# Performance work log

Hardware: AMD Instinct MI355X
Metric: run time of the kernel (lower is better)

Reference implementation:

```python
import jax, jax.numpy as jnp
import numpy as np

N = 50000      # nodes
E = 800000     # edges (avg degree 16)
IN = 128; HID = 128; OUT = 128; HEADS = 4
NEG_SLOPE = 0.2


def setup_inputs() -> dict:
    key = jax.random.key(0)
    ks = jax.random.split(key, 16)
    def glorot(k, shape):
        fan = shape[0] if len(shape) == 2 else int(np.prod(shape))
        return jax.random.normal(k, shape, jnp.float32) * np.float32(1.0 / np.sqrt(fan))
    C = HID // HEADS
    x = jax.random.normal(ks[0], (N, IN), jnp.float32)
    edge_index = jax.random.randint(ks[1], (2, E), 0, N, jnp.int32)
    return {
        "x": x, "edge_index": edge_index,
        "W1": glorot(ks[2], (IN, HID)),  "as1": glorot(ks[3], (HEADS, C)),  "ad1": glorot(ks[4], (HEADS, C)),  "b1": jnp.zeros((HID,), jnp.float32),
        "W2": glorot(ks[5], (HID, HID)), "as2": glorot(ks[6], (HEADS, C)),  "ad2": glorot(ks[7], (HEADS, C)),  "b2": jnp.zeros((HID,), jnp.float32),
        "W3": glorot(ks[8], (HID, OUT)), "as3": glorot(ks[9], (1, OUT)),    "ad3": glorot(ks[10], (1, OUT)),   "b3": jnp.zeros((OUT,), jnp.float32),
    }


def gat_conv(x, ei, W, a_src, a_dst, b, concat):
    # x: [N,Fin], ei: [2,E'] (self-loops included), W: [Fin, H*C], a_*: [H,C]
    n = x.shape[0]
    H, C = a_src.shape
    h = (x @ W).reshape(n, H, C)                         # [N,H,C]
    src, dst = ei[0], ei[1]
    alpha_s = jnp.einsum('nhc,hc->nh', h, a_src)         # [N,H]
    alpha_d = jnp.einsum('nhc,hc->nh', h, a_dst)
    e = jax.nn.leaky_relu(alpha_s[src] + alpha_d[dst], NEG_SLOPE)  # [E',H]
    # segment softmax over destination neighborhoods
    m = jax.ops.segment_max(e, dst, num_segments=n)      # [N,H]
    p = jnp.exp(e - m[dst])
    denom = jax.ops.segment_sum(p, dst, num_segments=n)  # [N,H]
    alpha = p / (denom[dst] + 1e-16)                     # [E',H]
    out = jax.ops.segment_sum(h[src] * alpha[:, :, None], dst, num_segments=n)  # [N,H,C]
    out = out.reshape(n, H * C) if concat else out.mean(axis=1)
    return out + b


def reference(x, edge_index, W1, as1, ad1, b1, W2, as2, ad2, b2, W3, as3, ad3, b3):
    n = x.shape[0]
    loops = jnp.arange(n, dtype=edge_index.dtype)
    ei = jnp.concatenate([edge_index, jnp.stack([loops, loops])], axis=1)  # add self-loops
    h = jax.nn.relu(gat_conv(x, ei, W1, as1, ad1, b1, True))   # dropout p=0 / eval: identity
    h = jax.nn.relu(gat_conv(h, ei, W2, as2, ad2, b2, True))
    return gat_conv(h, ei, W3, as3, ad3, b3, False)
```

## Files before the change

kernel.cpp:

```cpp
#include <hip/hip_runtime.h>
#include <hip/hip_bf16.h>
#include <math.h>

#define GB 512
#define SCB 2048

typedef __attribute__((ext_vector_type(8))) short bf16x8;
typedef __attribute__((ext_vector_type(4))) float f32x4;

__device__ __forceinline__ float lrelu(float v) { return fmaxf(v, 0.2f * v); }

__device__ __forceinline__ unsigned fenc(float f) {
    unsigned u = __float_as_uint(f);
    return (u & 0x80000000u) ? ~u : (u | 0x80000000u);
}
__device__ __forceinline__ float fdec(unsigned u) {
    return __uint_as_float((u & 0x80000000u) ? (u & 0x7FFFFFFFu) : ~u);
}
__device__ __forceinline__ unsigned short f2bf(float f) {
    union { __hip_bfloat16 b; unsigned short u; } cv;
    cv.b = __float2bfloat16(f);
    return cv.u;
}
__device__ __forceinline__ float bflo(unsigned u) { return __uint_as_float(u << 16); }
__device__ __forceinline__ float bfhi(unsigned u) { return __uint_as_float(u & 0xFFFF0000u); }


__global__ void setup_scatter(const float* __restrict__ x,
                              const float* __restrict__ W1, const float* __restrict__ W2,
                              const float* __restrict__ W3,
                              unsigned short* __restrict__ xb,
                              unsigned short* __restrict__ Wt1, unsigned short* __restrict__ Wt2,
                              unsigned short* __restrict__ Wt3,
                              int* __restrict__ cnt, unsigned short* __restrict__ srcs,
                              unsigned* __restrict__ gmax, unsigned short* __restrict__ hb,
                              const int* __restrict__ ei, int E,
                              int N, int GX, int pn) {
    int b = blockIdx.x, t = threadIdx.x;
    if (b < GX) {
        int i = b * 256 + t;
        if (i < N * 32) {
            float4 v = ((const float4*)x)[i];
            ushort4 o;
            o.x = f2bf(v.x); o.y = f2bf(v.y); o.z = f2bf(v.z); o.w = f2bf(v.w);
            ((ushort4*)xb)[i] = o;
        }
        if (i < N) srcs[(size_t)i << 6] = (unsigned short)i;
        if (i < 12) gmax[i] = fenc(-1e30f);
        if (i < 64) ((unsigned*)hb)[(size_t)N * 64 + i] = 0;
        return;
    }
    if (b < GX + 192) {
        int j = (b - GX) * 256 + t;
        int mm = j >> 14, e = j & 16383;
        const float* W = (mm == 0) ? W1 : (mm == 1) ? W2 : W3;
        unsigned short* Wt = (mm == 0) ? Wt1 : (mm == 1) ? Wt2 : Wt3;
        int k = e >> 7, c = e & 127;
        Wt[c * 128 + k] = f2bf(W[e]);
        return;
    }
    {
        int sb = b - GX - 192;
        int part = sb & 7;
        int chunk = sb >> 3;
        int stride = (SCB >> 3) * 256;
        int lo = part * pn, hi = min(lo + pn, N);
        for (int i = chunk * 256 + t; i < E; i += stride) {
            int d = ei[E + i];
            if (d >= lo && d < hi) {
                int idx = 1 + atomicAdd(&cnt[d], 1);
                if (idx < 64) srcs[((size_t)d << 6) + idx] = (unsigned short)ei[i];
            }
        }
    }
}


__device__ __forceinline__ void pad_body(int pb, int t, int* __restrict__ cnt,
                                         unsigned short* __restrict__ srcs, int N) {
    int n = pb * 256 + t;
    if (n >= N) return;
    int dr = cnt[n] + 1;
    if (dr > 64) dr = 64;
    int q = (dr + 3) >> 2;
    for (int k = dr; k < q * 4; k++) srcs[((size_t)n << 6) + k] = (unsigned short)N;
    cnt[n] = q;
}


template <int H>
__device__ __forceinline__ void gemm_body2(int wid, int nwaves, int wave,
                                           const unsigned short* __restrict__ xb,
                                           const unsigned short* __restrict__ Wt,
                                           const float* __restrict__ a_s,
                                           const float* __restrict__ a_d,
                                           unsigned short* __restrict__ hb,
                                           float* __restrict__ asb,
                                           float* __restrict__ adb,
                                           unsigned* __restrict__ gmax,
                                           float* __restrict__ wlds,
                                           float (*smax)[4], int N) {
    constexpr int HH = (H == 4) ? 4 : 1;
    int lane = threadIdx.x & 63;
    int lrow = lane & 15;
    int kg = lane >> 4;

    bf16x8 B[32];
#pragma unroll
    for (int ct = 0; ct < 8; ct++)
#pragma unroll
        for (int kk = 0; kk < 4; kk++)
            B[ct * 4 + kk] = *(const bf16x8*)(Wt + (size_t)(ct * 16 + lrow) * 128 + kk * 32 + kg * 8);

    int ntiles = (N + 15) >> 4;
    float wmax = -1e30f;

    bf16x8 A[4];
    {
        int tt = (wid < ntiles) ? wid : 0;
        int arow = min(tt * 16 + lrow, N - 1);
        const bf16x8* ap = (const bf16x8*)(xb + (size_t)arow * 128 + kg * 8);
        A[0] = ap[0]; A[1] = ap[4]; A[2] = ap[8]; A[3] = ap[12];
    }

    for (int t = wid; t < ntiles; t += nwaves) {
        bf16x8 An[4];
        {
            int tn = (t + nwaves < ntiles) ? t + nwaves : t;
            int arow = min(tn * 16 + lrow, N - 1);
            const bf16x8* ap = (const bf16x8*)(xb + (size_t)arow * 128 + kg * 8);
            An[0] = ap[0]; An[1] = ap[4]; An[2] = ap[8]; An[3] = ap[12];
        }
        f32x4 acc[8];
#pragma unroll
        for (int ct = 0; ct < 8; ct++) acc[ct] = (f32x4)0.f;
#pragma unroll
        for (int kk = 0; kk < 4; kk++)
#pragma unroll
            for (int ct = 0; ct < 8; ct++)
                acc[ct] = __builtin_amdgcn_mfma_f32_16x16x32_bf16(A[kk], B[ct * 4 + kk], acc[ct], 0, 0, 0);

#pragma unroll
        for (int ct = 0; ct < 8; ct++)
#pragma unroll
            for (int reg = 0; reg < 4; reg++)
                wlds[(kg * 4 + reg) * 132 + ct * 16 + lrow] = acc[ct][reg];

        const float* rp = wlds + lrow * 132 + kg * 32;
        const float* asp = a_s + kg * 32;
        const float* adp = a_d + kg * 32;
        float hv[32];
        float s = 0.f, d = 0.f;
#pragma unroll
        for (int q = 0; q < 8; q++) {
            float4 v = *(const float4*)(rp + q * 4);
            float4 av = *(const float4*)(asp + q * 4);
            float4 dv = *(const float4*)(adp + q * 4);
            hv[q * 4 + 0] = v.x; hv[q * 4 + 1] = v.y; hv[q * 4 + 2] = v.z; hv[q * 4 + 3] = v.w;
            s += v.x * av.x + v.y * av.y + v.z * av.z + v.w * av.w;
            d += v.x * dv.x + v.y * dv.y + v.z * dv.z + v.w * dv.w;
        }
        if (H == 1) {
            s += __shfl_xor(s, 16); s += __shfl_xor(s, 32);
            d += __shfl_xor(d, 16); d += __shfl_xor(d, 32);
        }
        int r = t * 16 + lrow;
        bool valid = r < N;
        if (valid) {
            if (H == 4) {
                asb[(size_t)r * 4 + kg] = s;
                adb[(size_t)r * 4 + kg] = d;
            } else if (kg == 0) {
                asb[r] = s;
                adb[r] = d;
            }
        }
        wmax = fmaxf(wmax, valid ? s : -1e30f);
        unsigned st[16];
#pragma unroll
        for (int q = 0; q < 16; q++)
            st[q] = (unsigned)f2bf(hv[2 * q]) | ((unsigned)f2bf(hv[2 * q + 1]) << 16);
        if (valid) {
            uint4* dst = (uint4*)(hb + (size_t)r * 128 + kg * 32);
            uint4 s0; s0.x = st[0];  s0.y = st[1];  s0.z = st[2];  s0.w = st[3];
            uint4 s1; s1.x = st[4];  s1.y = st[5];  s1.z = st[6];  s1.w = st[7];
            uint4 s2; s2.x = st[8];  s2.y = st[9];  s2.z = st[10]; s2.w = st[11];
            uint4 s3; s3.x = st[12]; s3.y = st[13]; s3.z = st[14]; s3.w = st[15];
            dst[0] = s0; dst[1] = s1; dst[2] = s2; dst[3] = s3;
        }
#pragma unroll
        for (int q = 0; q < 4; q++) A[q] = An[q];
    }

    if (H == 4) {
        wmax = fmaxf(wmax, __shfl_xor(wmax, 1));
        wmax = fmaxf(wmax, __shfl_xor(wmax, 2));
        wmax = fmaxf(wmax, __shfl_xor(wmax, 4));
        wmax = fmaxf(wmax, __shfl_xor(wmax, 8));
        if (lrow == 0) smax[wave][kg] = wmax;
    } else {
        wmax = fmaxf(wmax, __shfl_xor(wmax, 1));
        wmax = fmaxf(wmax, __shfl_xor(wmax, 2));
        wmax = fmaxf(wmax, __shfl_xor(wmax, 4));
        wmax = fmaxf(wmax, __shfl_xor(wmax, 8));
        wmax = fmaxf(wmax, __shfl_xor(wmax, 16));
        wmax = fmaxf(wmax, __shfl_xor(wmax, 32));
        if (lane == 0) smax[wave][0] = wmax;
    }
    __syncthreads();
    if (threadIdx.x < HH) {
        float m = fmaxf(fmaxf(smax[0][threadIdx.x], smax[1][threadIdx.x]),
                        fmaxf(smax[2][threadIdx.x], smax[3][threadIdx.x]));
        atomicMax(&gmax[threadIdx.x], fenc(m));
    }
    if (wid == 0 && threadIdx.x == 0) {
#pragma unroll
        for (int hd = 0; hd < HH; hd++) asb[(size_t)N * H + hd] = -1e30f;
    }
}


__global__ __launch_bounds__(256, 2) void gemm1_k(const unsigned short* __restrict__ xb,
                                                  const unsigned short* __restrict__ Wt,
                                                  const float* __restrict__ a_s,
                                                  const float* __restrict__ a_d,
                                                  unsigned short* __restrict__ hb,
                                                  float* __restrict__ asb,
                                                  float* __restrict__ adb,
                                                  unsigned* __restrict__ gmax, int N) {
    __shared__ float lds[4][16 * 132];
    __shared__ float smax[4][4];
    int wave = threadIdx.x >> 6;
    gemm_body2<4>(blockIdx.x * 4 + wave, GB * 4, wave, xb, Wt, a_s, a_d,
                  hb, asb, adb, gmax, lds[wave], smax, N);
}

__global__ __launch_bounds__(256, 2) void gemm2_pad(const unsigned short* __restrict__ xb,
                                                    const unsigned short* __restrict__ Wt,
                                                    const float* __restrict__ a_s,
                                                    const float* __restrict__ a_d,
                                                    unsigned short* __restrict__ hb,
                                                    float* __restrict__ asb,
                                                    float* __restrict__ adb,
                                                    unsigned* __restrict__ gmax,
                                                    int* __restrict__ cnt,
                                                    unsigned short* __restrict__ srcs, int N) {
    __shared__ float lds[4][16 * 132];
    __shared__ float smax[4][4];
    if ((int)blockIdx.x < GB) {
        int wave = threadIdx.x >> 6;
        gemm_body2<4>(blockIdx.x * 4 + wave, GB * 4, wave, xb, Wt, a_s, a_d,
                      hb, asb, adb, gmax, lds[wave], smax, N);
    } else {
        pad_body(blockIdx.x - GB, threadIdx.x, cnt, srcs, N);
    }
}

__global__ __launch_bounds__(256, 2) void gemm3_k(const unsigned short* __restrict__ xb,
                                                  const unsigned short* __restrict__ Wt,
                                                  const float* __restrict__ a_s,
                                                  const float* __restrict__ a_d,
                                                  unsigned short* __restrict__ hb,
                                                  float* __restrict__ asb,
                                                  float* __restrict__ adb,
                                                  unsigned* __restrict__ gmax, int N) {
    __shared__ float lds[4][16 * 132];
    __shared__ float smax[4][4];
    int wave = threadIdx.x >> 6;
    gemm_body2<1>(blockIdx.x * 4 + wave, GB * 4, wave, xb, Wt, a_s, a_d,
                  hb, asb, adb, gmax, lds[wave], smax, N);
}


template <int H, bool RELU, bool OUTBF, bool MASK>
__global__ __launch_bounds__(256) void aggregate10(const unsigned short* __restrict__ hb,
                                                   const unsigned short* __restrict__ srcs,
                                                   const int* __restrict__ qn,
                                                   const float* __restrict__ asb,
                                                   const float* __restrict__ adb,
                                                   const unsigned* __restrict__ gmax,
                                                   const float* __restrict__ bias,
                                                   void* __restrict__ outv, int N) {
    int n = (blockIdx.x * 256 + threadIdx.x) >> 4;
    if (n >= N) return;
    unsigned l = threadIdx.x & 15;
    unsigned ht = (H == 4) ? (l >> 2) : 0;
    int base = (threadIdx.x & 63) & ~15;
    float adn = adb[(unsigned)n * H + ht];
    float m = lrelu(fdec(gmax[ht]) + adn);
    const unsigned short* sp = srcs + ((size_t)n << 6);
    const uint4* hrow = (const uint4*)hb;
    int cv = qn[n];
    int nb, rem;
    if (MASK) {
        int dr = cv + 1;
        dr = min(dr, 64);
        nb = (dr + 3) >> 2;
        rem = dr - ((nb - 1) << 2);
    } else {
        nb = cv;
        rem = 4;
    }
    float a0 = 0.f, a1 = 0.f, a2 = 0.f, a3 = 0.f;
    float a4 = 0.f, a5 = 0.f, a6 = 0.f, a7 = 0.f, den = 0.f;

    ushort4 sq = *(const ushort4*)sp;
    uint4 u0 = hrow[(unsigned)sq.x * 16u + l];
    uint4 u1 = hrow[(unsigned)sq.y * 16u + l];
    uint4 u2 = hrow[(unsigned)sq.z * 16u + l];
    uint4 u3 = hrow[(unsigned)sq.w * 16u + l];
    for (int j = 0; j < nb; j++) {
        int jn = (j + 1 < nb) ? j + 1 : j;
        ushort4 sn = *(const ushort4*)(sp + jn * 4);
        uint4 v0 = hrow[(unsigned)sn.x * 16u + l];
        uint4 v1 = hrow[(unsigned)sn.y * 16u + l];
        uint4 v2 = hrow[(unsigned)sn.z * 16u + l];
        uint4 v3 = hrow[(unsigned)sn.w * 16u + l];
        unsigned sown = sp[j * 4 + (l & 3)];
        float e = asb[sown * H + ht];
        float pown = __expf(lrelu(e + adn) - m);
        float p0 = __shfl(pown, base + (int)ht * 4 + 0);
        float p1 = __shfl(pown, base + (int)ht * 4 + 1);
        float p2 = __shfl(pown, base + (int)ht * 4 + 2);
        float p3 = __shfl(pown, base + (int)ht * 4 + 3);
        if (MASK) {
            int limit = (j == nb - 1) ? rem : 4;
            p1 = (1 < limit) ? p1 : 0.f;
            p2 = (2 < limit) ? p2 : 0.f;
            p3 = (3 < limit) ? p3 : 0.f;
        }
        a0 += p0 * bflo(u0.x); a1 += p0 * bfhi(u0.x); a2 += p0 * bflo(u0.y); a3 += p0 * bfhi(u0.y);
        a4 += p0 * bflo(u0.z); a5 += p0 * bfhi(u0.z); a6 += p0 * bflo(u0.w); a7 += p0 * bfhi(u0.w);
        a0 += p1 * bflo(u1.x); a1 += p1 * bfhi(u1.x); a2 += p1 * bflo(u1.y); a3 += p1 * bfhi(u1.y);
        a4 += p1 * bflo(u1.z); a5 += p1 * bfhi(u1.z); a6 += p1 * bflo(u1.w); a7 += p1 * bfhi(u1.w);
        a0 += p2 * bflo(u2.x); a1 += p2 * bfhi(u2.x); a2 += p2 * bflo(u2.y); a3 += p2 * bfhi(u2.y);
        a4 += p2 * bflo(u2.z); a5 += p2 * bfhi(u2.z); a6 += p2 * bflo(u2.w); a7 += p2 * bfhi(u2.w);
        a0 += p3 * bflo(u3.x); a1 += p3 * bfhi(u3.x); a2 += p3 * bflo(u3.y); a3 += p3 * bfhi(u3.y);
        a4 += p3 * bflo(u3.z); a5 += p3 * bfhi(u3.z); a6 += p3 * bflo(u3.w); a7 += p3 * bfhi(u3.w);
        den += p0 + p1 + p2 + p3;
        sq = sn; u0 = v0; u1 = v1; u2 = v2; u3 = v3;
    }
    float inv = 1.f / (den + 1e-16f);
    unsigned c = l * 8;
    float4 bv0 = *(const float4*)&bias[c];
    float4 bv1 = *(const float4*)&bias[c + 4];
    float o0 = a0 * inv + bv0.x, o1 = a1 * inv + bv0.y;
    float o2 = a2 * inv + bv0.z, o3 = a3 * inv + bv0.w;
    float o4 = a4 * inv + bv1.x, o5 = a5 * inv + bv1.y;
    float o6 = a6 * inv + bv1.z, o7 = a7 * inv + bv1.w;
    if (RELU) {
        o0 = fmaxf(o0, 0.f); o1 = fmaxf(o1, 0.f); o2 = fmaxf(o2, 0.f); o3 = fmaxf(o3, 0.f);
        o4 = fmaxf(o4, 0.f); o5 = fmaxf(o5, 0.f); o6 = fmaxf(o6, 0.f); o7 = fmaxf(o7, 0.f);
    }
    if (OUTBF) {
        uint4 st;
        st.x = (unsigned)f2bf(o0) | ((unsigned)f2bf(o1) << 16);
        st.y = (unsigned)f2bf(o2) | ((unsigned)f2bf(o3) << 16);
        st.z = (unsigned)f2bf(o4) | ((unsigned)f2bf(o5) << 16);
        st.w = (unsigned)f2bf(o6) | ((unsigned)f2bf(o7) << 16);
        *(uint4*)&((unsigned short*)outv)[(size_t)n * 128 + c] = st;
    } else {
        float* op = (float*)outv + (size_t)n * 128 + c;
        float4 s0; s0.x = o0; s0.y = o1; s0.z = o2; s0.w = o3;
        float4 s1; s1.x = o4; s1.y = o5; s1.z = o6; s1.w = o7;
        *(float4*)op = s0;
        *(float4*)(op + 4) = s1;
    }
}


extern "C" void kernel_launch(void* const* d_in, const int* in_sizes, int n_in,
                              void* d_out, int out_size, void* d_ws, size_t ws_size,
                              hipStream_t stream) {
    const float* x   = (const float*)d_in[0];
    const int*   ei  = (const int*)d_in[1];
    const float* W1  = (const float*)d_in[2];
    const float* as1 = (const float*)d_in[3];
    const float* ad1 = (const float*)d_in[4];
    const float* b1  = (const float*)d_in[5];
    const float* W2  = (const float*)d_in[6];
    const float* as2 = (const float*)d_in[7];
    const float* ad2 = (const float*)d_in[8];
    const float* b2  = (const float*)d_in[9];
    const float* W3  = (const float*)d_in[10];
    const float* as3 = (const float*)d_in[11];
    const float* ad3 = (const float*)d_in[12];
    const float* b3  = (const float*)d_in[13];

    const int N = in_sizes[0] / 128;
    const int E = in_sizes[1] / 2;
    const int PN = (N + 7) / 8;

    char* w = (char*)d_ws;
    size_t woff = 0;
    auto alloc = [&](size_t bytes) -> void* {
        void* p = w + woff;
        woff = (woff + bytes + 255) & ~(size_t)255;
        return p;
    };
    int*      cnt  = (int*)alloc((size_t)(N + 1) * 4);
    unsigned short* srcs = (unsigned short*)alloc(((size_t)N * 64 + 64) * 2);
    float*    asb    = (float*)alloc((size_t)(N + 1) * 4 * 4);
    float*    adb    = (float*)alloc((size_t)(N + 1) * 4 * 4);
    unsigned* gmax   = (unsigned*)alloc(16 * 4);
    unsigned short* hb  = (unsigned short*)alloc((size_t)(N + 1) * 128 * 2);
    unsigned short* xb  = (unsigned short*)alloc((size_t)N * 128 * 2);
    unsigned short* Wt1 = (unsigned short*)alloc(128 * 128 * 2);
    unsigned short* Wt2 = (unsigned short*)alloc(128 * 128 * 2);
    unsigned short* Wt3 = (unsigned short*)alloc(128 * 128 * 2);
    float* outf = (float*)d_out;

    const int GX = (N * 32 + 255) / 256;
    const int ga = (N * 16 + 255) / 256;
    const int PB = (N + 255) / 256;

    hipMemsetAsync(cnt, 0, (size_t)N * 4, stream);

    setup_scatter<<<GX + 192 + SCB, 256, 0, stream>>>(x, W1, W2, W3, xb, Wt1, Wt2, Wt3,
                                                      cnt, srcs, gmax, hb, ei, E, N, GX, PN);

    gemm1_k<<<GB, 256, 0, stream>>>(xb, Wt1, as1, ad1, hb, asb, adb, gmax + 0, N);

    aggregate10<4, true, true, true><<<ga, 256, 0, stream>>>(hb, srcs, cnt, asb, adb,
                                                             gmax + 0, b1, xb, N);

    gemm2_pad<<<GB + PB, 256, 0, stream>>>(xb, Wt2, as2, ad2, hb, asb, adb, gmax + 4,
                                           cnt, srcs, N);

    aggregate10<4, true, true, false><<<ga, 256, 0, stream>>>(hb, srcs, cnt, asb, adb,
                                                              gmax + 4, b2, xb, N);

    gemm3_k<<<GB, 256, 0, stream>>>(xb, Wt3, as3, ad3, hb, asb, adb, gmax + 8, N);

    aggregate10<1, false, false, false><<<ga, 256, 0, stream>>>(hb, srcs, cnt, asb, adb,
                                                                gmax + 8, b3, outf, N);
}
```

Before: 223.6 us.

## Fuse fp32-to-bf16 input conversion into first GEMM and drop padding pass

Removes the separate x->bf16 conversion from the setup kernel. The first GEMM now loads fp32 x directly and converts A fragments in registers. It also drops the pad pass fused into gemm2 and uses masked tails in every aggregate call, plus the sentinel writes for hb/asb row N. This cuts a full read/write of x and some extra work, but doubles A-load bytes in gemm1 and adds masking to all aggregations. An unused 17MB workspace allocation is added.

```diff
diff --git a/kernel.cpp b/kernel.cpp
--- a/kernel.cpp
+++ b/kernel.cpp
@@ -26,32 +26,23 @@
 __device__ __forceinline__ float bfhi(unsigned u) { return __uint_as_float(u & 0xFFFF0000u); }
 
 
-__global__ void setup_scatter(const float* __restrict__ x,
-                              const float* __restrict__ W1, const float* __restrict__ W2,
+__global__ void setup_scatter(const float* __restrict__ W1, const float* __restrict__ W2,
                               const float* __restrict__ W3,
-                              unsigned short* __restrict__ xb,
                               unsigned short* __restrict__ Wt1, unsigned short* __restrict__ Wt2,
                               unsigned short* __restrict__ Wt3,
                               int* __restrict__ cnt, unsigned short* __restrict__ srcs,
-                              unsigned* __restrict__ gmax, unsigned short* __restrict__ hb,
+                              unsigned* __restrict__ gmax,
                               const int* __restrict__ ei, int E,
-                              int N, int GX, int pn) {
+                              int N, int GA, int pn) {
     int b = blockIdx.x, t = threadIdx.x;
-    if (b < GX) {
+    if (b < GA) {
         int i = b * 256 + t;
-        if (i < N * 32) {
-            float4 v = ((const float4*)x)[i];
-            ushort4 o;
-            o.x = f2bf(v.x); o.y = f2bf(v.y); o.z = f2bf(v.z); o.w = f2bf(v.w);
-            ((ushort4*)xb)[i] = o;
-        }
         if (i < N) srcs[(size_t)i << 6] = (unsigned short)i;
         if (i < 12) gmax[i] = fenc(-1e30f);
-        if (i < 64) ((unsigned*)hb)[(size_t)N * 64 + i] = 0;
         return;
     }
-    if (b < GX + 192) {
-        int j = (b - GX) * 256 + t;
+    if (b < GA + 192) {
+        int j = (b - GA) * 256 + t;
         int mm = j >> 14, e = j & 16383;
         const float* W = (mm == 0) ? W1 : (mm == 1) ? W2 : W3;
         unsigned short* Wt = (mm == 0) ? Wt1 : (mm == 1) ? Wt2 : Wt3;
@@ -60,7 +51,7 @@
         return;
     }
     {
-        int sb = b - GX - 192;
+        int sb = b - GA - 192;
         int part = sb & 7;
         int chunk = sb >> 3;
         int stride = (SCB >> 3) * 256;
@@ -76,21 +67,20 @@
 }
 
 
-__device__ __forceinline__ void pad_body(int pb, int t, int* __restrict__ cnt,
-                                         unsigned short* __restrict__ srcs, int N) {
-    int n = pb * 256 + t;
-    if (n >= N) return;
-    int dr = cnt[n] + 1;
-    if (dr > 64) dr = 64;
-    int q = (dr + 3) >> 2;
-    for (int k = dr; k < q * 4; k++) srcs[((size_t)n << 6) + k] = (unsigned short)N;
-    cnt[n] = q;
-}
-
-
-template <int H>
+__device__ __forceinline__ bf16x8 frag_f32(const float* p) {
+    float4 a = *(const float4*)p;
+    float4 b = *(const float4*)(p + 4);
+    bf16x8 r;
+    r[0] = (short)f2bf(a.x); r[1] = (short)f2bf(a.y);
+    r[2] = (short)f2bf(a.z); r[3] = (short)f2bf(a.w);
+    r[4] = (short)f2bf(b.x); r[5] = (short)f2bf(b.y);
+    r[6] = (short)f2bf(b.z); r[7] = (short)f2bf(b.w);
+    return r;
+}
+
+template <int H, bool AFP32>
 __device__ __forceinline__ void gemm_body2(int wid, int nwaves, int wave,
-                                           const unsigned short* __restrict__ xb,
+                                           const void* __restrict__ xin,
                                            const unsigned short* __restrict__ Wt,
                                            const float* __restrict__ a_s,
                                            const float* __restrict__ a_d,
@@ -115,22 +105,26 @@
     int ntiles = (N + 15) >> 4;
     float wmax = -1e30f;
 
+    auto loadA = [&](int tile, bf16x8* A) {
+        int arow = min(tile * 16 + lrow, N - 1);
+        if (AFP32) {
+            const float* xp = (const float*)xin + (size_t)arow * 128 + kg * 8;
+#pragma unroll
+            for (int kk = 0; kk < 4; kk++) A[kk] = frag_f32(xp + kk * 32);
+        } else {
+            const bf16x8* ap = (const bf16x8*)((const unsigned short*)xin + (size_t)arow * 128 + kg * 8);
+#pragma unroll
+            for (int kk = 0; kk < 4; kk++) A[kk] = ap[kk * 4];
+        }
+    };
+
     bf16x8 A[4];
-    {
-        int tt = (wid < ntiles) ? wid : 0;
-        int arow = min(tt * 16 + lrow, N - 1);
-        const bf16x8* ap = (const bf16x8*)(xb + (size_t)arow * 128 + kg * 8);
-        A[0] = ap[0]; A[1] = ap[4]; A[2] = ap[8]; A[3] = ap[12];
-    }
+    loadA((wid < ntiles) ? wid : 0, A);
 
     for (int t = wid; t < ntiles; t += nwaves) {
         bf16x8 An[4];
-        {
-            int tn = (t + nwaves < ntiles) ? t + nwaves : t;
-            int arow = min(tn * 16 + lrow, N - 1);
-            const bf16x8* ap = (const bf16x8*)(xb + (size_t)arow * 128 + kg * 8);
-            An[0] = ap[0]; An[1] = ap[4]; An[2] = ap[8]; An[3] = ap[12];
-        }
+        loadA((t + nwaves < ntiles) ? t + nwaves : t, An);
+
         f32x4 acc[8];
 #pragma unroll
         for (int ct = 0; ct < 8; ct++) acc[ct] = (f32x4)0.f;
@@ -213,14 +207,10 @@
                         fmaxf(smax[2][threadIdx.x], smax[3][threadIdx.x]));
         atomicMax(&gmax[threadIdx.x], fenc(m));
     }
-    if (wid == 0 && threadIdx.x == 0) {
-#pragma unroll
-        for (int hd = 0; hd < HH; hd++) asb[(size_t)N * H + hd] = -1e30f;
-    }
-}
-
-
-__global__ __launch_bounds__(256, 2) void gemm1_k(const unsigned short* __restrict__ xb,
+}
+
+
+__global__ __launch_bounds__(256, 2) void gemm1_k(const float* __restrict__ x,
                                                   const unsigned short* __restrict__ Wt,
                                                   const float* __restrict__ a_s,
                                                   const float* __restrict__ a_d,
@@ -231,29 +221,23 @@
     __shared__ float lds[4][16 * 132];
     __shared__ float smax[4][4];
     int wave = threadIdx.x >> 6;
-    gemm_body2<4>(blockIdx.x * 4 + wave, GB * 4, wave, xb, Wt, a_s, a_d,
-                  hb, asb, adb, gmax, lds[wave], smax, N);
-}
-
-__global__ __launch_bounds__(256, 2) void gemm2_pad(const unsigned short* __restrict__ xb,
-                                                    const unsigned short* __restrict__ Wt,
-                                                    const float* __restrict__ a_s,
-                                                    const float* __restrict__ a_d,
-                                                    unsigned short* __restrict__ hb,
-                                                    float* __restrict__ asb,
-                                                    float* __restrict__ adb,
-                                                    unsigned* __restrict__ gmax,
-                                                    int* __restrict__ cnt,
-                                                    unsigned short* __restrict__ srcs, int N) {
+    gemm_body2<4, true>(blockIdx.x * 4 + wave, GB * 4, wave, x, Wt, a_s, a_d,
+                        hb, asb, adb, gmax, lds[wave], smax, N);
+}
+
+__global__ __launch_bounds__(256, 2) void gemm2_k(const unsigned short* __restrict__ xb,
+                                                  const unsigned short* __restrict__ Wt,
+                                                  const float* __restrict__ a_s,
+                                                  const float* __restrict__ a_d,
+                                                  unsigned short* __restrict__ hb,
+                                                  float* __restrict__ asb,
+                                                  float* __restrict__ adb,
+                                                  unsigned* __restrict__ gmax, int N) {
     __shared__ float lds[4][16 * 132];
     __shared__ float smax[4][4];
-    if ((int)blockIdx.x < GB) {
-        int wave = threadIdx.x >> 6;
-        gemm_body2<4>(blockIdx.x * 4 + wave, GB * 4, wave, xb, Wt, a_s, a_d,
-                      hb, asb, adb, gmax, lds[wave], smax, N);
-    } else {
-        pad_body(blockIdx.x - GB, threadIdx.x, cnt, srcs, N);
-    }
+    int wave = threadIdx.x >> 6;
+    gemm_body2<4, false>(blockIdx.x * 4 + wave, GB * 4, wave, xb, Wt, a_s, a_d,
+                         hb, asb, adb, gmax, lds[wave], smax, N);
 }
 
 __global__ __launch_bounds__(256, 2) void gemm3_k(const unsigned short* __restrict__ xb,
@@ -267,15 +251,15 @@
     __shared__ float lds[4][16 * 132];
     __shared__ float smax[4][4];
     int wave = threadIdx.x >> 6;
-    gemm_body2<1>(blockIdx.x * 4 + wave, GB * 4, wave, xb, Wt, a_s, a_d,
-                  hb, asb, adb, gmax, lds[wave], smax, N);
-}
-
-
-template <int H, bool RELU, bool OUTBF, bool MASK>
+    gemm_body2<1, false>(blockIdx.x * 4 + wave, GB * 4, wave, xb, Wt, a_s, a_d,
+                         hb, asb, adb, gmax, lds[wave], smax, N);
+}
+
+
+template <int H, bool RELU, bool OUTBF>
 __global__ __launch_bounds__(256) void aggregate10(const unsigned short* __restrict__ hb,
                                                    const unsigned short* __restrict__ srcs,
-                                                   const int* __restrict__ qn,
+                                                   const int* __restrict__ cnt,
                                                    const float* __restrict__ asb,
                                                    const float* __restrict__ adb,
                                                    const unsigned* __restrict__ gmax,
@@ -290,17 +274,10 @@
     float m = lrelu(fdec(gmax[ht]) + adn);
     const unsigned short* sp = srcs + ((size_t)n << 6);
     const uint4* hrow = (const uint4*)hb;
-    int cv = qn[n];
-    int nb, rem;
-    if (MASK) {
-        int dr = cv + 1;
-        dr = min(dr, 64);
-        nb = (dr + 3) >> 2;
-        rem = dr - ((nb - 1) << 2);
-    } else {
-        nb = cv;
-        rem = 4;
-    }
+    int dr = cnt[n] + 1;
+    dr = min(dr, 64);
+    int nb = (dr + 3) >> 2;
+    int rem = dr - ((nb - 1) << 2);
     float a0 = 0.f, a1 = 0.f, a2 = 0.f, a3 = 0.f;
     float a4 = 0.f, a5 = 0.f, a6 = 0.f, a7 = 0.f, den = 0.f;
 
@@ -323,12 +300,10 @@
         float p1 = __shfl(pown, base + (int)ht * 4 + 1);
         float p2 = __shfl(pown, base + (int)ht * 4 + 2);
         float p3 = __shfl(pown, base + (int)ht * 4 + 3);
-        if (MASK) {
-            int limit = (j == nb - 1) ? rem : 4;
-            p1 = (1 < limit) ? p1 : 0.f;
-            p2 = (2 < limit) ? p2 : 0.f;
-            p3 = (3 < limit) ? p3 : 0.f;
-        }
+        int limit = (j == nb - 1) ? rem : 4;
+        p1 = (1 < limit) ? p1 : 0.f;
+        p2 = (2 < limit) ? p2 : 0.f;
+        p3 = (3 < limit) ? p3 : 0.f;
         a0 += p0 * bflo(u0.x); a1 += p0 * bfhi(u0.x); a2 += p0 * bflo(u0.y); a3 += p0 * bfhi(u0.y);
         a4 += p0 * bflo(u0.z); a5 += p0 * bfhi(u0.z); a6 += p0 * bflo(u0.w); a7 += p0 * bfhi(u0.w);
         a0 += p1 * bflo(u1.x); a1 += p1 * bfhi(u1.x); a2 += p1 * bflo(u1.y); a3 += p1 * bfhi(u1.y);
@@ -408,30 +383,29 @@
     unsigned short* Wt1 = (unsigned short*)alloc(128 * 128 * 2);
     unsigned short* Wt2 = (unsigned short*)alloc(128 * 128 * 2);
     unsigned short* Wt3 = (unsigned short*)alloc(128 * 128 * 2);
+    (void)alloc((size_t)17 * 1024 * 1024);
     float* outf = (float*)d_out;
 
-    const int GX = (N * 32 + 255) / 256;
+    const int GA = (N + 255) / 256;
     const int ga = (N * 16 + 255) / 256;
-    const int PB = (N + 255) / 256;
 
     hipMemsetAsync(cnt, 0, (size_t)N * 4, stream);
 
-    setup_scatter<<<GX + 192 + SCB, 256, 0, stream>>>(x, W1, W2, W3, xb, Wt1, Wt2, Wt3,
-                                                      cnt, srcs, gmax, hb, ei, E, N, GX, PN);
-
-    gemm1_k<<<GB, 256, 0, stream>>>(xb, Wt1, as1, ad1, hb, asb, adb, gmax + 0, N);
-
-    aggregate10<4, true, true, true><<<ga, 256, 0, stream>>>(hb, srcs, cnt, asb, adb,
-                                                             gmax + 0, b1, xb, N);
-
-    gemm2_pad<<<GB + PB, 256, 0, stream>>>(xb, Wt2, as2, ad2, hb, asb, adb, gmax + 4,
-                                           cnt, srcs, N);
-
-    aggregate10<4, true, true, false><<<ga, 256, 0, stream>>>(hb, srcs, cnt, asb, adb,
-                                                              gmax + 4, b2, xb, N);
+    setup_scatter<<<GA + 192 + SCB, 256, 0, stream>>>(W1, W2, W3, Wt1, Wt2, Wt3,
+                                                      cnt, srcs, gmax, ei, E, N, GA, PN);
+
+    gemm1_k<<<GB, 256, 0, stream>>>(x, Wt1, as1, ad1, hb, asb, adb, gmax + 0, N);
+
+    aggregate10<4, true, true><<<ga, 256, 0, stream>>>(hb, srcs, cnt, asb, adb,
+                                                       gmax + 0, b1, xb, N);
+
+    gemm2_k<<<GB, 256, 0, stream>>>(xb, Wt2, as2, ad2, hb, asb, adb, gmax + 4, N);
+
+    aggregate10<4, true, true><<<ga, 256, 0, stream>>>(hb, srcs, cnt, asb, adb,
+                                                       gmax + 4, b2, xb, N);
 
     gemm3_k<<<GB, 256, 0, stream>>>(xb, Wt3, as3, ad3, hb, asb, adb, gmax + 8, N);
 
-    aggregate10<1, false, false, false><<<ga, 256, 0, stream>>>(hb, srcs, cnt, asb, adb,
-                                                                gmax + 8, b3, outf, N);
-}
+    aggregate10<1, false, false><<<ga, 256, 0, stream>>>(hb, srcs, cnt, asb, adb,
+                                                         gmax + 8, b3, outf, N);
+}
```

New measurement: 223.2 us. No clear change (-0.2%).
